# Kernel optimization log

Measured on AMD Instinct MI355X. Metric: run time of the kernel, lower is better.

Reference implementation:

```python
import jax, jax.numpy as jnp
import numpy as np

B, T, E, H = 2, 4096, 1024, 16
D = E // H
EPS = 1e-6


def setup_inputs() -> dict:
    key = jax.random.key(0)
    ks = jax.random.split(key, 9)
    s = 1.0 / np.sqrt(E)
    return {
        "x": jax.random.normal(ks[0], (B, T, E), dtype=jnp.float32),
        "wq": jax.random.uniform(ks[1], (E, E), jnp.float32, -s, s),
        "bq": jax.random.uniform(ks[2], (E,), jnp.float32, -s, s),
        "wk": jax.random.uniform(ks[3], (E, E), jnp.float32, -s, s),
        "bk": jax.random.uniform(ks[4], (E,), jnp.float32, -s, s),
        "wv": jax.random.uniform(ks[5], (E, E), jnp.float32, -s, s),
        "bv": jax.random.uniform(ks[6], (E,), jnp.float32, -s, s),
        "wo": jax.random.uniform(ks[7], (E, E), jnp.float32, -s, s),
        "bo": jax.random.uniform(ks[8], (E,), jnp.float32, -s, s),
    }


def _feature_map(x):
    # elu(x) + 1
    return jnp.where(x > 0, x + 1.0, jnp.exp(x))


def reference(x, wq, bq, wk, bk, wv, bv, wo, bo):
    b, t, e = x.shape
    q = _feature_map(x @ wq + bq).reshape(b, t, H, D)
    k = _feature_map(x @ wk + bk).reshape(b, t, H, D)
    v = (x @ wv + bv).reshape(b, t, H, D)

    # time-major for the recurrence: [T, B, H, D]
    qT = jnp.moveaxis(q, 1, 0)
    kT = jnp.moveaxis(k, 1, 0)
    vT = jnp.moveaxis(v, 1, 0)

    S0 = jnp.zeros((b, H, D, D), dtype=x.dtype)  # running sum of k \otimes v
    z0 = jnp.zeros((b, H, D), dtype=x.dtype)     # running sum of k

    def step(carry, qkv):
        S, z = carry
        qt, kt, vt = qkv
        S = S + jnp.einsum('bhd,bhe->bhde', kt, vt)
        z = z + kt
        num = jnp.einsum('bhd,bhde->bhe', qt, S)
        den = jnp.einsum('bhd,bhd->bh', qt, z)[..., None] + EPS
        return (S, z), num / den

    _, outT = jax.lax.scan(step, (S0, z0), (qT, kT, vT))  # [T, B, H, D]
    out = jnp.moveaxis(outT, 0, 1).reshape(b, t, e)
    return out @ wo + bo
```

## Files before the change

### kernel.cpp

```cpp
#include <hip/hip_runtime.h>
#include <hip/hip_bf16.h>
#include <cstdint>
#include <cstddef>

#define B_   2
#define T_   4096
#define E_   1024
#define H_   16
#define D_   64
#define M_   (B_ * T_)
#define KDIM 1024
#define NDIM 1024
#define EPSC 1e-6f
#define CT   128
#define NC   (T_ / CT)

typedef __attribute__((ext_vector_type(8))) short bf16x8;
typedef __attribute__((ext_vector_type(4))) float f32x4;

__device__ __forceinline__ float bf2f(uint32_t u) {
    union { uint32_t u; float f; } x; x.u = u << 16; return x.f;
}
__device__ __forceinline__ unsigned short f2bf(float f) {
    union { float f; uint32_t u; } x; x.f = f;
    uint32_t r = x.u + 0x7fffu + ((x.u >> 16) & 1u);
    return (unsigned short)(r >> 16);
}
__device__ __forceinline__ void gload16(const void* g, void* l) {
    __builtin_amdgcn_global_load_lds(
        (const __attribute__((address_space(1))) void*)g,
        (__attribute__((address_space(3))) void*)l, 16, 0, 0);
}

__global__ __launch_bounds__(256) void prep(
    const float* __restrict__ x, unsigned short* __restrict__ xb,
    const float* __restrict__ w0, const float* __restrict__ w1,
    const float* __restrict__ w2, const float* __restrict__ w3,
    unsigned short* __restrict__ o0, unsigned short* __restrict__ o1,
    unsigned short* __restrict__ o2, unsigned short* __restrict__ o3)
{
    const int t = threadIdx.x;
    if (blockIdx.z == 4) {
        const int bi = blockIdx.y * 16 + blockIdx.x;
        const float4* p = (const float4*)x;
#pragma unroll
        for (int j = 0; j < 16; ++j) {
            const int i = bi * 256 + t + j * 65536;
            float4 a = p[i * 2], b = p[i * 2 + 1];
            ushort4 q0 = make_ushort4(f2bf(a.x), f2bf(a.y), f2bf(a.z), f2bf(a.w));
            ushort4 q1 = make_ushort4(f2bf(b.x), f2bf(b.y), f2bf(b.z), f2bf(b.w));
            *(ushort4*)&xb[(size_t)i * 8] = q0;
            *(ushort4*)&xb[(size_t)i * 8 + 4] = q1;
        }
        return;
    }
    const float* src; unsigned short* dst;
    switch (blockIdx.z) {
        case 0: src = w0; dst = o0; break;
        case 1: src = w1; dst = o1; break;
        case 2: src = w2; dst = o2; break;
        default: src = w3; dst = o3; break;
    }
    __shared__ float tile[64][65];
    const int tx = t & 63, ty = t >> 6;
    const int r0 = blockIdx.y * 64, c0 = blockIdx.x * 64;
#pragma unroll
    for (int i = 0; i < 16; ++i)
        tile[ty + i * 4][tx] = src[(size_t)(r0 + ty + i * 4) * KDIM + c0 + tx];
    __syncthreads();
#pragma unroll
    for (int i = 0; i < 16; ++i)
        dst[(size_t)(c0 + ty + i * 4) * KDIM + r0 + tx] = f2bf(tile[tx][ty + i * 4]);
}

template <int MODE>
__global__ __launch_bounds__(512, 1) void gemm_tb(
    const unsigned short* __restrict__ A,
    const unsigned short* __restrict__ Wt,
    const float* __restrict__ bq, const float* __restrict__ bk,
    const float* __restrict__ bv,
    unsigned short* __restrict__ qb,  unsigned short* __restrict__ kb,
    unsigned short* __restrict__ ktb, unsigned short* __restrict__ vtb,
    float* __restrict__ outf)
{
    __shared__ char lds[147456];

    const int tid  = threadIdx.x;
    const int lane = tid & 63;
    const int w    = tid >> 6;
    const int wm   = w >> 1;
    const int wn   = w & 1;
    const int lo   = lane & 15, hi = lane >> 4;

    int bx, by;
    if (MODE == 0) {
        const int orig = blockIdx.x;
        const int swz  = (orig & 7) * 96 + (orig >> 3);
        bx = swz % 24;
        by = swz / 24;
    } else {
        const int orig = blockIdx.x;
        bx = orig & 7;
        by = orig >> 3;
    }
    const int row0 = by * 256;
    const int col0 = bx * 128;

    int sr, skE;
    { int X = tid * 16; int Y = X ^ (((X >> 7) & 7) << 4);
      sr = Y >> 7; skE = (Y & 127) >> 1; }
    const unsigned short* pa = A  + (size_t)(row0 + sr) * KDIM + skE;
    const unsigned short* pb = Wt + (size_t)(col0 + sr) * KDIM + skE;

#define STG(t, da, db) {                                                      \
    { char* d_ = (da) + tid * 16;                                             \
      _Pragma("unroll") for (int ch = 0; ch < 4; ++ch)                        \
        gload16(pa + (size_t)ch * 64 * KDIM + (t) * 64, d_ + ch * 8192); }    \
    { char* d_ = (db) + tid * 16;                                             \
      _Pragma("unroll") for (int ch = 0; ch < 2; ++ch)                        \
        gload16(pb + (size_t)ch * 64 * KDIM + (t) * 64, d_ + ch * 8192); } }

    const int koff0 = (hi * 16)       ^ ((lane & 7) << 4);
    const int koff1 = (64 + hi * 16)  ^ ((lane & 7) << 4);

    f32x4 acc[4][4] = {};
    const int NT = KDIM / 64;

    char* pA0 = lds;           char* pB0 = lds + 98304;
    char* pA1 = lds + 32768;   char* pB1 = lds + 114688;
    char* pA2 = lds + 65536;   char* pB2 = lds + 131072;

    STG(0, pA0, pB0);
    STG(1, pA1, pB1);
    asm volatile("s_waitcnt vmcnt(6)" ::: "memory");
    __builtin_amdgcn_s_barrier();

    for (int t = 0; t < NT; ++t) {
        if (t + 2 < NT) STG(t + 2, pA2, pB2);

        bf16x8 af[4][2], bfr[4][2];
#pragma unroll
        for (int m = 0; m < 4; ++m) {
            const char* p = pA0 + (wm * 64 + m * 16 + lo) * 128;
            af[m][0] = *(const bf16x8*)(p + koff0);
            af[m][1] = *(const bf16x8*)(p + koff1);
        }
#pragma unroll
        for (int n = 0; n < 4; ++n) {
            const char* p = pB0 + (wn * 64 + n * 16 + lo) * 128;
            bfr[n][0] = *(const bf16x8*)(p + koff0);
            bfr[n][1] = *(const bf16x8*)(p + koff1);
        }
        __builtin_amdgcn_s_setprio(1);
#pragma unroll
        for (int kk = 0; kk < 2; ++kk)
#pragma unroll
            for (int m = 0; m < 4; ++m)
#pragma unroll
                for (int n = 0; n < 4; ++n)
                    acc[m][n] = __builtin_amdgcn_mfma_f32_16x16x32_bf16(
                        af[m][kk], bfr[n][kk], acc[m][n], 0, 0, 0);
        __builtin_amdgcn_s_setprio(0);

        if (t + 2 < NT) { asm volatile("s_waitcnt vmcnt(6)" ::: "memory"); }
        else            { asm volatile("s_waitcnt vmcnt(0)" ::: "memory"); }
        asm volatile("s_waitcnt lgkmcnt(0)" ::: "memory");
        __builtin_amdgcn_s_barrier();

        char* ta = pA0; pA0 = pA1; pA1 = pA2; pA2 = ta;
        char* tb = pB0; pB0 = pB1; pB1 = pB2; pB2 = tb;
    }
#undef STG

    if (MODE == 1) {
#pragma unroll
        for (int n = 0; n < 4; ++n) {
            const int col = col0 + wn * 64 + n * 16 + lo;
            const float bval = bq[col];
#pragma unroll
            for (int m = 0; m < 4; ++m) {
                const int rbase = row0 + wm * 64 + m * 16 + hi * 4;
#pragma unroll
                for (int j = 0; j < 4; ++j)
                    outf[(size_t)(rbase + j) * NDIM + col] = acc[m][n][j] + bval;
            }
        }
        return;
    }

    unsigned short* ep = (unsigned short*)lds;
    const int matid = bx >> 3;
    const float* bias = (matid == 0) ? bq : (matid == 1) ? bk : bv;
#pragma unroll
    for (int n = 0; n < 4; ++n) {
        const int lcol = wn * 64 + n * 16 + lo;
        const float bval = bias[(bx & 7) * 128 + lcol];
#pragma unroll
        for (int m = 0; m < 4; ++m) {
            const int lr0 = wm * 64 + m * 16 + hi * 4;
#pragma unroll
            for (int j = 0; j < 4; ++j) {
                float v = acc[m][n][j] + bval;
                if (matid <= 1) v = (v > 0.f) ? (v + 1.f) : __expf(v);
                ep[(lr0 + j) * 136 + lcol] = f2bf(v);
            }
        }
    }
    __syncthreads();

    const int b   = row0 >> 12;
    const int tg0 = row0 & (T_ - 1);
    const int h0  = (bx & 7) * 2;

    if (matid <= 1) {
        unsigned short* dst0 = (matid == 0) ? qb : kb;
#pragma unroll
        for (int it = 0; it < 8; ++it) {
            const int vid = it * 512 + tid;
            const int head = vid >> 11;
            const int rem = vid & 2047;
            const int tr = rem >> 3, c8 = rem & 7;
            uint4 v = *(const uint4*)&ep[tr * 136 + head * 64 + c8 * 8];
            *(uint4*)&dst0[((size_t)((b * H_ + h0 + head) * T_) + tg0 + tr) * D_
                           + c8 * 8] = v;
        }
    }
    if (matid >= 1) {
        unsigned short* dstT = (matid == 1) ? ktb : vtb;
#pragma unroll
        for (int it = 0; it < 8; ++it) {
            const int vid = it * 512 + tid;
            const int head = vid >> 11;
            const int rem = vid & 2047;
            const int d = rem & 63, t8 = rem >> 6;
            unsigned short vals[8];
#pragma unroll
            for (int i = 0; i < 8; ++i)
                vals[i] = ep[(t8 * 8 + i) * 136 + head * 64 + d];
            *(uint4*)&dstT[((size_t)((b * H_ + h0 + head) * D_) + d) * T_
                           + tg0 + t8 * 8] = *(const uint4*)vals;
        }
    }
}

__global__ __launch_bounds__(256) void chunk_sums_mfma(
    const unsigned short* __restrict__ Kt,
    const unsigned short* __restrict__ Vt,
    unsigned short* __restrict__ Sl,
    unsigned short* __restrict__ Zl)
{
    const int tid = threadIdx.x, lane = tid & 63, w = tid >> 6;
    const int lo = lane & 15, hi = lane >> 4;
    const int cid = blockIdx.x, bh = cid >> 5, c = cid & 31, t0 = c * CT;
    const unsigned short* kT = Kt + (size_t)bh * 64 * T_ + t0;
    const unsigned short* vT = Vt + (size_t)bh * 64 * T_ + t0;

    const bf16x8 ones8 = {0x3F80, 0x3F80, 0x3F80, 0x3F80,
                          0x3F80, 0x3F80, 0x3F80, 0x3F80};
    f32x4 acc[5] = {};
#pragma unroll
    for (int kt = 0; kt < 4; ++kt) {
        bf16x8 af = *(const bf16x8*)&kT[(size_t)(w * 16 + lo) * T_ + kt * 32 + hi * 8];
        bf16x8 bfr[5];
#pragma unroll
        for (int et = 0; et < 4; ++et)
            bfr[et] = *(const bf16x8*)&vT[(size_t)(et * 16 + lo) * T_ + kt * 32 + hi * 8];
        bfr[4] = ones8;
#pragma unroll
        for (int et = 0; et < 5; ++et)
            acc[et] = __builtin_amdgcn_mfma_f32_16x16x32_bf16(af, bfr[et], acc[et], 0, 0, 0);
    }
    unsigned short* sO = Sl + (size_t)cid * 4096;
    const int d0 = w * 16 + hi * 4;
#pragma unroll
    for (int et = 0; et < 4; ++et) {
        const int e = et * 16 + lo;
        ushort4 pk = make_ushort4(f2bf(acc[et][0]), f2bf(acc[et][1]),
                                  f2bf(acc[et][2]), f2bf(acc[et][3]));
        *(ushort4*)&sO[e * 64 + d0] = pk;
    }
    if (lo == 0) {
        ushort4 pk = make_ushort4(f2bf(acc[4][0]), f2bf(acc[4][1]),
                                  f2bf(acc[4][2]), f2bf(acc[4][3]));
        *(ushort4*)&Zl[(size_t)cid * 64 + d0] = pk;
    }
}

__global__ __launch_bounds__(256) void chunk_scan_bf(
    unsigned short* __restrict__ S, unsigned short* __restrict__ Z)
{
    const int bh = blockIdx.y;
    const int f0 = blockIdx.x * 512 + threadIdx.x * 2;
    float a0 = 0.f, a1 = 0.f;
    unsigned short* base = S + (size_t)bh * NC * 4096 + f0;
    for (int c = 0; c < NC; ++c) {
        uint32_t* p = (uint32_t*)(base + (size_t)c * 4096);
        uint32_t v = *p;
        float c0 = bf2f(v & 0xffffu), c1 = bf2f(v >> 16);
        *p = (uint32_t)f2bf(a0) | ((uint32_t)f2bf(a1) << 16);
        a0 += c0; a1 += c1;
    }
    if (blockIdx.x == 0 && threadIdx.x < 32) {
        float b0 = 0.f, b1 = 0.f;
        unsigned short* zb = Z + (size_t)bh * NC * 64 + threadIdx.x * 2;
        for (int c = 0; c < NC; ++c) {
            uint32_t* p = (uint32_t*)(zb + (size_t)c * 64);
            uint32_t v = *p;
            float c0 = bf2f(v & 0xffffu), c1 = bf2f(v >> 16);
            *p = (uint32_t)f2bf(b0) | ((uint32_t)f2bf(b1) << 16);
            b0 += c0; b1 += c1;
        }
    }
}

__global__ __launch_bounds__(256) void chunk_attn_mfma(
    const unsigned short* __restrict__ Qb,
    const unsigned short* __restrict__ Kb,
    const unsigned short* __restrict__ Vt,
    const unsigned short* __restrict__ SpT,
    const unsigned short* __restrict__ Zp,
    unsigned short* __restrict__ att)
{
    __shared__ unsigned short lds[128 * 128];

    const int tid = threadIdx.x;
    const int lane = tid & 63;
    const int w = tid >> 6;
    const int lo = lane & 15, hi = lane >> 4;
    const int cid = blockIdx.x;
    const int bh = cid >> 5, c = cid & 31;
    const int t0 = c * CT;

    const unsigned short* qB = Qb + ((size_t)bh * T_ + t0) * 64;
    const unsigned short* kB = Kb + ((size_t)bh * T_ + t0) * 64;
    const unsigned short* vB = Vt + (size_t)bh * 64 * T_ + t0;
    const unsigned short* sB = SpT + (size_t)cid * 4096;
    const unsigned short* zB = Zp + (size_t)cid * 64;

    bf16x8 ka[2][2];
#pragma unroll
    for (int si = 0; si < 2; ++si)
#pragma unroll
        for (int kt = 0; kt < 2; ++kt)
            ka[si][kt] = *(const bf16x8*)&kB[(w * 32 + si * 16 + lo) * 64 + kt * 32 + hi * 8];

    f32x4 pacc[2][8] = {};
#pragma unroll
    for (int ti = 0; ti < 8; ++ti) {
        if (ti >= 2 * w) {
#pragma unroll
            for (int kt = 0; kt < 2; ++kt) {
                bf16x8 qf = *(const bf16x8*)&qB[(ti * 16 + lo) * 64 + kt * 32 + hi * 8];
                pacc[0][ti] = __builtin_amdgcn_mfma_f32_16x16x32_bf16(
                    ka[0][kt], qf, pacc[0][ti], 0, 0, 0);
                if (ti >= 2 * w + 1)
                    pacc[1][ti] = __builtin_amdgcn_mfma_f32_16x16x32_bf16(
                        ka[1][kt], qf, pacc[1][ti], 0, 0, 0);
            }
        }
    }
#pragma unroll
    for (int ti = 0; ti < 8; ++ti) {
        if (ti >= 2 * w) {
            const int t = ti * 16 + lo;
#pragma unroll
            for (int si = 0; si < 2; ++si) {
                const int s0 = w * 32 + si * 16 + hi * 4;
                ushort4 pk;
                unsigned short* pe = (unsigned short*)&pk;
#pragma unroll
                for (int j = 0; j < 4; ++j)
                    pe[j] = (s0 + j <= t) ? f2bf(pacc[si][ti][j]) : (unsigned short)0;
                *(ushort4*)((char*)lds + t * 256 + ((s0 * 2) ^ ((t & 7) << 4))) = pk;
            }
        }
    }
    __syncthreads();

    const bf16x8 ones8 = {0x3F80, 0x3F80, 0x3F80, 0x3F80,
                          0x3F80, 0x3F80, 0x3F80, 0x3F80};
    f32x4 acc[2][5] = {};
#pragma unroll
    for (int kt = 0; kt < 6; ++kt) {
        const int skt = kt - 2;
        if (kt < 2 || skt <= w) {
            bf16x8 bfr[5];
            if (kt < 2) {
#pragma unroll
                for (int et = 0; et < 4; ++et)
                    bfr[et] = *(const bf16x8*)&sB[(et * 16 + lo) * 64 + kt * 32 + hi * 8];
                bfr[4] = *(const bf16x8*)&zB[kt * 32 + hi * 8];
            } else {
#pragma unroll
                for (int et = 0; et < 4; ++et)
                    bfr[et] = *(const bf16x8*)&vB[(size_t)(et * 16 + lo) * T_ + skt * 32 + hi * 8];
                bfr[4] = ones8;
            }
#pragma unroll
            for (int m = 0; m < 2; ++m) {
                const int t = w * 32 + m * 16 + lo;
                bf16x8 af;
                if (kt < 2)
                    af = *(const bf16x8*)&qB[t * 64 + kt * 32 + hi * 8];
                else
                    af = *(const bf16x8*)((char*)lds + t * 256 +
                         (((skt * 32 + hi * 8) * 2) ^ ((t & 7) << 4)));
#pragma unroll
                for (int et = 0; et < 5; ++et)
                    acc[m][et] = __builtin_amdgcn_mfma_f32_16x16x32_bf16(
                        af, bfr[et], acc[m][et], 0, 0, 0);
            }
        }
    }

    __syncthreads();
#pragma unroll
    for (int m = 0; m < 2; ++m) {
#pragma unroll
        for (int j = 0; j < 4; ++j) {
            const int t = w * 32 + m * 16 + hi * 4 + j;
            const float rden = 1.f / (acc[m][4][j] + EPSC);
#pragma unroll
            for (int et = 0; et < 4; ++et) {
                const int e = et * 16 + lo;
                *(unsigned short*)((char*)lds + t * 144 + e * 2) =
                    f2bf(acc[m][et][j] * rden);
            }
        }
    }
    __syncthreads();
    const int b = bh >> 4, h = bh & 15;
#pragma unroll
    for (int r = 0; r < 4; ++r) {
        const int vid = tid + r * 256;
        const int t = vid >> 3, eg = vid & 7;
        uint4 val = *(const uint4*)((const char*)lds + t * 144 + eg * 16);
        *(uint4*)&att[(size_t)(b * T_ + t0 + t) * E_ + h * 64 + eg * 8] = val;
    }
}

extern "C" void kernel_launch(void* const* d_in, const int* in_sizes, int n_in,
                              void* d_out, int out_size, void* d_ws, size_t ws_size,
                              hipStream_t stream)
{
    const float* x  = (const float*)d_in[0];
    const float* wq = (const float*)d_in[1];
    const float* bq = (const float*)d_in[2];
    const float* wk = (const float*)d_in[3];
    const float* bk = (const float*)d_in[4];
    const float* wv = (const float*)d_in[5];
    const float* bv = (const float*)d_in[6];
    const float* wo = (const float*)d_in[7];
    const float* bo = (const float*)d_in[8];
    float* out = (float*)d_out;

    char* ws = (char*)d_ws;
    unsigned short* qb  = (unsigned short*)(ws);
    unsigned short* kb  = (unsigned short*)(ws + (size_t)16 * 1024 * 1024);
    unsigned short* ktb = (unsigned short*)(ws + (size_t)32 * 1024 * 1024);
    unsigned short* vtb = (unsigned short*)(ws + (size_t)48 * 1024 * 1024);
    unsigned short* xb  = (unsigned short*)(ws + (size_t)64 * 1024 * 1024);
    unsigned short* attb = xb;
    unsigned short* Sl  = (unsigned short*)(ws + (size_t)80 * 1024 * 1024);
    unsigned short* Zl  = (unsigned short*)(ws + (size_t)88 * 1024 * 1024);
    unsigned short* wqT = (unsigned short*)(ws + (size_t)88 * 1024 * 1024 + 128 * 1024);
    unsigned short* wkT = wqT + (size_t)KDIM * NDIM;
    unsigned short* wvT = wkT + (size_t)KDIM * NDIM;
    unsigned short* woT = wvT + (size_t)KDIM * NDIM;

    prep<<<dim3(16, 16, 5), 256, 0, stream>>>(x, xb, wq, wk, wv, wo,
                                              wqT, wkT, wvT, woT);

    gemm_tb<0><<<768, 512, 0, stream>>>(xb, wqT, bq, bk, bv,
                                        qb, kb, ktb, vtb, nullptr);

    chunk_sums_mfma<<<B_ * H_ * NC, 256, 0, stream>>>(ktb, vtb, Sl, Zl);
    chunk_scan_bf<<<dim3(8, B_ * H_), 256, 0, stream>>>(Sl, Zl);
    chunk_attn_mfma<<<B_ * H_ * NC, 256, 0, stream>>>(qb, kb, vtb, Sl, Zl, attb);

    gemm_tb<1><<<256, 512, 0, stream>>>(attb, woT, bo, nullptr, nullptr,
                                        nullptr, nullptr, nullptr, nullptr, out);
}
```

Measured before the change: 165.8 us.

## Use 256x256 tiles with 8-phase interleaved pipeline for QKV projection GEMM

Replaces the templated QKV GEMM with a dedicated kernel using 256x256 output tiles, eight warps in a 2x4 grid and double-buffered LDS. The main loop is split into four MFMA phases interleaved with partial global-to-LDS loads and barriers, and launch bounds now request two blocks per CU. The goal is more arithmetic per loaded byte and better overlap of loads with matrix math in the largest GEMM. The epilogue is done in two halves to fit LDS, and the output GEMM is split into its own plain kernel. Risks include register pressure from 32 accumulators per lane with occupancy 2, and the extra barriers.

```diff
diff --git a/kernel.cpp b/kernel.cpp
--- a/kernel.cpp
+++ b/kernel.cpp
@@ -73,15 +73,189 @@
         dst[(size_t)(c0 + ty + i * 4) * KDIM + r0 + tx] = f2bf(tile[tx][ty + i * 4]);
 }
 
-template <int MODE>
-__global__ __launch_bounds__(512, 1) void gemm_tb(
+__global__ __launch_bounds__(512, 2) void gemm_qkv8p(
     const unsigned short* __restrict__ A,
     const unsigned short* __restrict__ Wt,
     const float* __restrict__ bq, const float* __restrict__ bk,
     const float* __restrict__ bv,
     unsigned short* __restrict__ qb,  unsigned short* __restrict__ kb,
-    unsigned short* __restrict__ ktb, unsigned short* __restrict__ vtb,
-    float* __restrict__ outf)
+    unsigned short* __restrict__ ktb, unsigned short* __restrict__ vtb)
+{
+    __shared__ char lds[131072];
+
+    const int tid  = threadIdx.x;
+    const int lane = tid & 63;
+    const int w    = tid >> 6;
+    const int wm   = w >> 2;
+    const int wn   = w & 3;
+    const int lo   = lane & 15, hi = lane >> 4;
+
+    const int orig = blockIdx.x;
+    const int swz  = (orig & 7) * 48 + (orig >> 3);
+    const int bx = swz % 12;
+    const int by = swz / 12;
+    const int row0 = by * 256;
+    const int col0 = bx * 256;
+
+    const unsigned short* srcA[2][2];
+    const unsigned short* srcB[2][2];
+#pragma unroll
+    for (int h = 0; h < 2; ++h)
+#pragma unroll
+        for (int j = 0; j < 2; ++j) {
+            int X = j * 8192 + tid * 16;
+            int Y = X ^ (((X >> 7) & 7) << 4);
+            int lr = Y >> 7, ke = (Y & 127) >> 1;
+            srcA[h][j] = A  + (size_t)(row0 + h * 128 + lr) * KDIM + ke;
+            srcB[h][j] = Wt + (size_t)(col0 + h * 128 + lr) * KDIM + ke;
+        }
+
+#define STG_A(t, h) { char* d_ = lds + ((t) & 1) * 65536 + (h) * 16384 + tid * 16; \
+        gload16(srcA[h][0] + (t) * 64, d_); gload16(srcA[h][1] + (t) * 64, d_ + 8192); }
+#define STG_B(t, h) { char* d_ = lds + ((t) & 1) * 65536 + 32768 + (h) * 16384 + tid * 16; \
+        gload16(srcB[h][0] + (t) * 64, d_); gload16(srcB[h][1] + (t) * 64, d_ + 8192); }
+
+    const int koff0 = (hi * 16)      ^ ((lo & 7) << 4);
+    const int koff1 = (64 + hi * 16) ^ ((lo & 7) << 4);
+
+    f32x4  acc[8][4] = {};
+    bf16x8 af[4][2], bfr[4][2];
+    const int NT = KDIM / 64;
+
+#define MFMA16(mb, nb) {                                                      \
+    _Pragma("unroll") for (int kk = 0; kk < 2; ++kk)                          \
+    _Pragma("unroll") for (int m = 0; m < 4; ++m)                             \
+    _Pragma("unroll") for (int n = 0; n < 2; ++n)                             \
+        acc[(mb) + m][(nb) + n] = __builtin_amdgcn_mfma_f32_16x16x32_bf16(    \
+            af[m][kk], bfr[(nb) + n][kk], acc[(mb) + m][(nb) + n], 0, 0, 0); }
+
+    STG_A(0, 0); STG_A(0, 1); STG_B(0, 0); STG_B(0, 1);
+    STG_A(1, 0); STG_A(1, 1);
+    asm volatile("s_waitcnt vmcnt(4)" ::: "memory");
+    __builtin_amdgcn_s_barrier();
+
+    for (int t = 0; t < NT; ++t) {
+        const char* bb = lds + (t & 1) * 65536;
+        const char* bA = bb + wm * 16384;
+        const char* bB = bb + 32768 + (wn >> 1) * 16384;
+        const int lrb = (wn & 1) * 64;
+
+        if (t + 1 < NT) STG_B(t + 1, 0);
+#pragma unroll
+        for (int m = 0; m < 4; ++m) {
+            const char* p = bA + (m * 16 + lo) * 128;
+            af[m][0] = *(const bf16x8*)(p + koff0);
+            af[m][1] = *(const bf16x8*)(p + koff1);
+        }
+#pragma unroll
+        for (int n = 0; n < 4; ++n) {
+            const char* p = bB + (lrb + n * 16 + lo) * 128;
+            bfr[n][0] = *(const bf16x8*)(p + koff0);
+            bfr[n][1] = *(const bf16x8*)(p + koff1);
+        }
+        __builtin_amdgcn_s_barrier();
+        asm volatile("s_waitcnt lgkmcnt(0)" ::: "memory");
+        __builtin_amdgcn_s_setprio(1);
+        MFMA16(0, 0);
+        __builtin_amdgcn_s_setprio(0);
+        __builtin_amdgcn_s_barrier();
+
+        if (t + 1 < NT) STG_B(t + 1, 1);
+        __builtin_amdgcn_s_barrier();
+        __builtin_amdgcn_s_setprio(1);
+        MFMA16(0, 2);
+        __builtin_amdgcn_s_setprio(0);
+        __builtin_amdgcn_s_barrier();
+
+#pragma unroll
+        for (int m = 0; m < 4; ++m) {
+            const char* p = bA + ((m + 4) * 16 + lo) * 128;
+            af[m][0] = *(const bf16x8*)(p + koff0);
+            af[m][1] = *(const bf16x8*)(p + koff1);
+        }
+        __builtin_amdgcn_s_barrier();
+        asm volatile("s_waitcnt lgkmcnt(0)" ::: "memory");
+        __builtin_amdgcn_s_setprio(1);
+        MFMA16(4, 0);
+        __builtin_amdgcn_s_setprio(0);
+        __builtin_amdgcn_s_barrier();
+
+        if (t + 2 < NT) { STG_A(t + 2, 0); STG_A(t + 2, 1); }
+        __builtin_amdgcn_s_setprio(1);
+        MFMA16(4, 2);
+        __builtin_amdgcn_s_setprio(0);
+        if (t + 2 < NT)      asm volatile("s_waitcnt vmcnt(4)" ::: "memory");
+        else if (t + 1 < NT) asm volatile("s_waitcnt vmcnt(0)" ::: "memory");
+        __builtin_amdgcn_s_barrier();
+    }
+#undef STG_A
+#undef STG_B
+#undef MFMA16
+
+    unsigned short* ep = (unsigned short*)lds;
+    const int matid = bx >> 2;
+    const float* bias = (matid == 0) ? bq : (matid == 1) ? bk : bv;
+    const int b   = row0 >> 12;
+    const int tg0 = row0 & (T_ - 1);
+    const int h0  = (bx & 3) * 4;
+
+#pragma unroll
+    for (int ph = 0; ph < 2; ++ph) {
+        if (wm == ph) {
+#pragma unroll
+            for (int n = 0; n < 4; ++n) {
+                const int col = wn * 64 + n * 16 + lo;
+                const float bval = bias[(bx & 3) * 256 + col];
+#pragma unroll
+                for (int m = 0; m < 8; ++m) {
+#pragma unroll
+                    for (int j = 0; j < 4; ++j) {
+                        float v = acc[m][n][j] + bval;
+                        if (matid <= 1) v = (v > 0.f) ? (v + 1.f) : __expf(v);
+                        ep[(m * 16 + hi * 4 + j) * 272 + col] = f2bf(v);
+                    }
+                }
+            }
+        }
+        __syncthreads();
+
+        if (matid <= 1) {
+            unsigned short* dst0 = (matid == 0) ? qb : kb;
+#pragma unroll
+            for (int it = 0; it < 8; ++it) {
+                const int vid = it * 512 + tid;
+                const int r = vid >> 5;
+                const int lc8 = vid & 31;
+                const int head = lc8 >> 3, d8 = lc8 & 7;
+                uint4 v = *(const uint4*)&ep[r * 272 + lc8 * 8];
+                *(uint4*)&dst0[((size_t)((b * H_ + h0 + head) * T_)
+                                + tg0 + ph * 128 + r) * D_ + d8 * 8] = v;
+            }
+        }
+        if (matid >= 1) {
+            unsigned short* dstT = (matid == 1) ? ktb : vtb;
+#pragma unroll
+            for (int it = 0; it < 8; ++it) {
+                const int vid = it * 512 + tid;
+                const int d = vid & 63;
+                const int idx = vid >> 6;
+                const int head = idx >> 4, t8 = idx & 15;
+                unsigned short vals[8];
+#pragma unroll
+                for (int i = 0; i < 8; ++i)
+                    vals[i] = ep[(t8 * 8 + i) * 272 + head * 64 + d];
+                *(uint4*)&dstT[((size_t)((b * H_ + h0 + head) * D_) + d) * T_
+                               + tg0 + ph * 128 + t8 * 8] = *(const uint4*)vals;
+            }
+        }
+        __syncthreads();
+    }
+}
+
+__global__ __launch_bounds__(512, 1) void gemm_out_tb(
+    const unsigned short* __restrict__ A,
+    const unsigned short* __restrict__ Wt,
+    const float* __restrict__ bias, float* __restrict__ outf)
 {
     __shared__ char lds[147456];
 
@@ -92,17 +266,9 @@
     const int wn   = w & 1;
     const int lo   = lane & 15, hi = lane >> 4;
 
-    int bx, by;
-    if (MODE == 0) {
-        const int orig = blockIdx.x;
-        const int swz  = (orig & 7) * 96 + (orig >> 3);
-        bx = swz % 24;
-        by = swz / 24;
-    } else {
-        const int orig = blockIdx.x;
-        bx = orig & 7;
-        by = orig >> 3;
-    }
+    const int orig = blockIdx.x;
+    const int bx = orig & 7;
+    const int by = orig >> 3;
     const int row0 = by * 256;
     const int col0 = bx * 128;
 
@@ -172,73 +338,16 @@
     }
 #undef STG
 
-    if (MODE == 1) {
-#pragma unroll
-        for (int n = 0; n < 4; ++n) {
-            const int col = col0 + wn * 64 + n * 16 + lo;
-            const float bval = bq[col];
-#pragma unroll
-            for (int m = 0; m < 4; ++m) {
-                const int rbase = row0 + wm * 64 + m * 16 + hi * 4;
-#pragma unroll
-                for (int j = 0; j < 4; ++j)
-                    outf[(size_t)(rbase + j) * NDIM + col] = acc[m][n][j] + bval;
-            }
-        }
-        return;
-    }
-
-    unsigned short* ep = (unsigned short*)lds;
-    const int matid = bx >> 3;
-    const float* bias = (matid == 0) ? bq : (matid == 1) ? bk : bv;
 #pragma unroll
     for (int n = 0; n < 4; ++n) {
-        const int lcol = wn * 64 + n * 16 + lo;
-        const float bval = bias[(bx & 7) * 128 + lcol];
+        const int col = col0 + wn * 64 + n * 16 + lo;
+        const float bval = bias[col];
 #pragma unroll
         for (int m = 0; m < 4; ++m) {
-            const int lr0 = wm * 64 + m * 16 + hi * 4;
-#pragma unroll
-            for (int j = 0; j < 4; ++j) {
-                float v = acc[m][n][j] + bval;
-                if (matid <= 1) v = (v > 0.f) ? (v + 1.f) : __expf(v);
-                ep[(lr0 + j) * 136 + lcol] = f2bf(v);
-            }
-        }
-    }
-    __syncthreads();
-
-    const int b   = row0 >> 12;
-    const int tg0 = row0 & (T_ - 1);
-    const int h0  = (bx & 7) * 2;
-
-    if (matid <= 1) {
-        unsigned short* dst0 = (matid == 0) ? qb : kb;
-#pragma unroll
-        for (int it = 0; it < 8; ++it) {
-            const int vid = it * 512 + tid;
-            const int head = vid >> 11;
-            const int rem = vid & 2047;
-            const int tr = rem >> 3, c8 = rem & 7;
-            uint4 v = *(const uint4*)&ep[tr * 136 + head * 64 + c8 * 8];
-            *(uint4*)&dst0[((size_t)((b * H_ + h0 + head) * T_) + tg0 + tr) * D_
-                           + c8 * 8] = v;
-        }
-    }
-    if (matid >= 1) {
-        unsigned short* dstT = (matid == 1) ? ktb : vtb;
-#pragma unroll
-        for (int it = 0; it < 8; ++it) {
-            const int vid = it * 512 + tid;
-            const int head = vid >> 11;
-            const int rem = vid & 2047;
-            const int d = rem & 63, t8 = rem >> 6;
-            unsigned short vals[8];
-#pragma unroll
-            for (int i = 0; i < 8; ++i)
-                vals[i] = ep[(t8 * 8 + i) * 136 + head * 64 + d];
-            *(uint4*)&dstT[((size_t)((b * H_ + h0 + head) * D_) + d) * T_
-                           + tg0 + t8 * 8] = *(const uint4*)vals;
+            const int rbase = row0 + wm * 64 + m * 16 + hi * 4;
+#pragma unroll
+            for (int j = 0; j < 4; ++j)
+                outf[(size_t)(rbase + j) * NDIM + col] = acc[m][n][j] + bval;
         }
     }
 }
@@ -471,13 +580,11 @@
     prep<<<dim3(16, 16, 5), 256, 0, stream>>>(x, xb, wq, wk, wv, wo,
                                               wqT, wkT, wvT, woT);
 
-    gemm_tb<0><<<768, 512, 0, stream>>>(xb, wqT, bq, bk, bv,
-                                        qb, kb, ktb, vtb, nullptr);
+    gemm_qkv8p<<<384, 512, 0, stream>>>(xb, wqT, bq, bk, bv, qb, kb, ktb, vtb);
 
     chunk_sums_mfma<<<B_ * H_ * NC, 256, 0, stream>>>(ktb, vtb, Sl, Zl);
     chunk_scan_bf<<<dim3(8, B_ * H_), 256, 0, stream>>>(Sl, Zl);
     chunk_attn_mfma<<<B_ * H_ * NC, 256, 0, stream>>>(qb, kb, vtb, Sl, Zl, attb);
 
-    gemm_tb<1><<<256, 512, 0, stream>>>(attb, woT, bo, nullptr, nullptr,
-                                        nullptr, nullptr, nullptr, nullptr, out);
-}
+    gemm_out_tb<<<256, 512, 0, stream>>>(attb, woT, bo, out);
+}
```

Measured after the change: 175.5 us. 1.06x slower.

## Replace LDS-staged triple-buffered GEMM with direct global-to-register MFMA GEMM

Applied to the files above, without the earlier changes.

The QKV and output projection GEMMs stop staging A and W tiles through LDS with a triple-buffered global_load_lds pipeline. Each wave now loads its MFMA fragments straight from global memory into registers, on 128x128 tiles with 256 threads, which doubles the block count and allows more blocks per CU. The aim is to drop LDS traffic, barriers and waitcnt stalls and lean on L1/L2 and occupancy to hide latency. The cost is that operands shared across waves are no longer reused through LDS, so global and cache traffic rise, and the loop has no explicit prefetch.

```diff
diff --git a/kernel.cpp b/kernel.cpp
--- a/kernel.cpp
+++ b/kernel.cpp
@@ -26,11 +26,6 @@
     uint32_t r = x.u + 0x7fffu + ((x.u >> 16) & 1u);
     return (unsigned short)(r >> 16);
 }
-__device__ __forceinline__ void gload16(const void* g, void* l) {
-    __builtin_amdgcn_global_load_lds(
-        (const __attribute__((address_space(1))) void*)g,
-        (__attribute__((address_space(3))) void*)l, 16, 0, 0);
-}
 
 __global__ __launch_bounds__(256) void prep(
     const float* __restrict__ x, unsigned short* __restrict__ xb,
@@ -74,7 +69,7 @@
 }
 
 template <int MODE>
-__global__ __launch_bounds__(512, 1) void gemm_tb(
+__global__ __launch_bounds__(256) void gemm_reg(
     const unsigned short* __restrict__ A,
     const unsigned short* __restrict__ Wt,
     const float* __restrict__ bq, const float* __restrict__ bk,
@@ -83,75 +78,54 @@
     unsigned short* __restrict__ ktb, unsigned short* __restrict__ vtb,
     float* __restrict__ outf)
 {
-    __shared__ char lds[147456];
+    __shared__ unsigned short ep[(MODE == 0) ? 128 * 136 : 16];
 
     const int tid  = threadIdx.x;
     const int lane = tid & 63;
     const int w    = tid >> 6;
-    const int wm   = w >> 1;
-    const int wn   = w & 1;
+    const int wr   = w >> 1;
+    const int wc   = w & 1;
     const int lo   = lane & 15, hi = lane >> 4;
 
     int bx, by;
     if (MODE == 0) {
         const int orig = blockIdx.x;
-        const int swz  = (orig & 7) * 96 + (orig >> 3);
+        const int swz  = (orig & 7) * 192 + (orig >> 3);
         bx = swz % 24;
         by = swz / 24;
     } else {
         const int orig = blockIdx.x;
-        bx = orig & 7;
-        by = orig >> 3;
-    }
-    const int row0 = by * 256;
+        const int swz  = (orig & 7) * 64 + (orig >> 3);
+        bx = swz & 7;
+        by = swz >> 3;
+    }
+    const int row0 = by * 128;
     const int col0 = bx * 128;
 
-    int sr, skE;
-    { int X = tid * 16; int Y = X ^ (((X >> 7) & 7) << 4);
-      sr = Y >> 7; skE = (Y & 127) >> 1; }
-    const unsigned short* pa = A  + (size_t)(row0 + sr) * KDIM + skE;
-    const unsigned short* pb = Wt + (size_t)(col0 + sr) * KDIM + skE;
-
-#define STG(t, da, db) {                                                      \
-    { char* d_ = (da) + tid * 16;                                             \
-      _Pragma("unroll") for (int ch = 0; ch < 4; ++ch)                        \
-        gload16(pa + (size_t)ch * 64 * KDIM + (t) * 64, d_ + ch * 8192); }    \
-    { char* d_ = (db) + tid * 16;                                             \
-      _Pragma("unroll") for (int ch = 0; ch < 2; ++ch)                        \
-        gload16(pb + (size_t)ch * 64 * KDIM + (t) * 64, d_ + ch * 8192); } }
-
-    const int koff0 = (hi * 16)       ^ ((lane & 7) << 4);
-    const int koff1 = (64 + hi * 16)  ^ ((lane & 7) << 4);
+    const unsigned short* aP[4];
+    const unsigned short* bP[4];
+#pragma unroll
+    for (int m = 0; m < 4; ++m)
+        aP[m] = A + (size_t)(row0 + wr * 64 + m * 16 + lo) * KDIM + hi * 8;
+#pragma unroll
+    for (int n = 0; n < 4; ++n)
+        bP[n] = Wt + (size_t)(col0 + wc * 64 + n * 16 + lo) * KDIM + hi * 8;
 
     f32x4 acc[4][4] = {};
-    const int NT = KDIM / 64;
-
-    char* pA0 = lds;           char* pB0 = lds + 98304;
-    char* pA1 = lds + 32768;   char* pB1 = lds + 114688;
-    char* pA2 = lds + 65536;   char* pB2 = lds + 131072;
-
-    STG(0, pA0, pB0);
-    STG(1, pA1, pB1);
-    asm volatile("s_waitcnt vmcnt(6)" ::: "memory");
-    __builtin_amdgcn_s_barrier();
-
-    for (int t = 0; t < NT; ++t) {
-        if (t + 2 < NT) STG(t + 2, pA2, pB2);
-
+
+    for (int t = 0; t < KDIM / 64; ++t) {
         bf16x8 af[4][2], bfr[4][2];
+        const int ko = t * 64;
 #pragma unroll
         for (int m = 0; m < 4; ++m) {
-            const char* p = pA0 + (wm * 64 + m * 16 + lo) * 128;
-            af[m][0] = *(const bf16x8*)(p + koff0);
-            af[m][1] = *(const bf16x8*)(p + koff1);
+            af[m][0] = *(const bf16x8*)(aP[m] + ko);
+            af[m][1] = *(const bf16x8*)(aP[m] + ko + 32);
         }
 #pragma unroll
         for (int n = 0; n < 4; ++n) {
-            const char* p = pB0 + (wn * 64 + n * 16 + lo) * 128;
-            bfr[n][0] = *(const bf16x8*)(p + koff0);
-            bfr[n][1] = *(const bf16x8*)(p + koff1);
-        }
-        __builtin_amdgcn_s_setprio(1);
+            bfr[n][0] = *(const bf16x8*)(bP[n] + ko);
+            bfr[n][1] = *(const bf16x8*)(bP[n] + ko + 32);
+        }
 #pragma unroll
         for (int kk = 0; kk < 2; ++kk)
 #pragma unroll
@@ -160,26 +134,16 @@
                 for (int n = 0; n < 4; ++n)
                     acc[m][n] = __builtin_amdgcn_mfma_f32_16x16x32_bf16(
                         af[m][kk], bfr[n][kk], acc[m][n], 0, 0, 0);
-        __builtin_amdgcn_s_setprio(0);
-
-        if (t + 2 < NT) { asm volatile("s_waitcnt vmcnt(6)" ::: "memory"); }
-        else            { asm volatile("s_waitcnt vmcnt(0)" ::: "memory"); }
-        asm volatile("s_waitcnt lgkmcnt(0)" ::: "memory");
-        __builtin_amdgcn_s_barrier();
-
-        char* ta = pA0; pA0 = pA1; pA1 = pA2; pA2 = ta;
-        char* tb = pB0; pB0 = pB1; pB1 = pB2; pB2 = tb;
-    }
-#undef STG
+    }
 
     if (MODE == 1) {
 #pragma unroll
         for (int n = 0; n < 4; ++n) {
-            const int col = col0 + wn * 64 + n * 16 + lo;
+            const int col = col0 + wc * 64 + n * 16 + lo;
             const float bval = bq[col];
 #pragma unroll
             for (int m = 0; m < 4; ++m) {
-                const int rbase = row0 + wm * 64 + m * 16 + hi * 4;
+                const int rbase = row0 + wr * 64 + m * 16 + hi * 4;
 #pragma unroll
                 for (int j = 0; j < 4; ++j)
                     outf[(size_t)(rbase + j) * NDIM + col] = acc[m][n][j] + bval;
@@ -188,16 +152,15 @@
         return;
     }
 
-    unsigned short* ep = (unsigned short*)lds;
     const int matid = bx >> 3;
     const float* bias = (matid == 0) ? bq : (matid == 1) ? bk : bv;
 #pragma unroll
     for (int n = 0; n < 4; ++n) {
-        const int lcol = wn * 64 + n * 16 + lo;
+        const int lcol = wc * 64 + n * 16 + lo;
         const float bval = bias[(bx & 7) * 128 + lcol];
 #pragma unroll
         for (int m = 0; m < 4; ++m) {
-            const int lr0 = wm * 64 + m * 16 + hi * 4;
+            const int lr0 = wr * 64 + m * 16 + hi * 4;
 #pragma unroll
             for (int j = 0; j < 4; ++j) {
                 float v = acc[m][n][j] + bval;
@@ -216,9 +179,9 @@
         unsigned short* dst0 = (matid == 0) ? qb : kb;
 #pragma unroll
         for (int it = 0; it < 8; ++it) {
-            const int vid = it * 512 + tid;
-            const int head = vid >> 11;
-            const int rem = vid & 2047;
+            const int vid = it * 256 + tid;
+            const int head = vid >> 10;
+            const int rem = vid & 1023;
             const int tr = rem >> 3, c8 = rem & 7;
             uint4 v = *(const uint4*)&ep[tr * 136 + head * 64 + c8 * 8];
             *(uint4*)&dst0[((size_t)((b * H_ + h0 + head) * T_) + tg0 + tr) * D_
@@ -229,10 +192,10 @@
         unsigned short* dstT = (matid == 1) ? ktb : vtb;
 #pragma unroll
         for (int it = 0; it < 8; ++it) {
-            const int vid = it * 512 + tid;
-            const int head = vid >> 11;
-            const int rem = vid & 2047;
-            const int d = rem & 63, t8 = rem >> 6;
+            const int vid = it * 256 + tid;
+            const int d = vid & 63;
+            const int idx = vid >> 6;
+            const int head = idx >> 4, t8 = idx & 15;
             unsigned short vals[8];
 #pragma unroll
             for (int i = 0; i < 8; ++i)
@@ -471,13 +434,13 @@
     prep<<<dim3(16, 16, 5), 256, 0, stream>>>(x, xb, wq, wk, wv, wo,
                                               wqT, wkT, wvT, woT);
 
-    gemm_tb<0><<<768, 512, 0, stream>>>(xb, wqT, bq, bk, bv,
-                                        qb, kb, ktb, vtb, nullptr);
+    gemm_reg<0><<<1536, 256, 0, stream>>>(xb, wqT, bq, bk, bv,
+                                          qb, kb, ktb, vtb, nullptr);
 
     chunk_sums_mfma<<<B_ * H_ * NC, 256, 0, stream>>>(ktb, vtb, Sl, Zl);
     chunk_scan_bf<<<dim3(8, B_ * H_), 256, 0, stream>>>(Sl, Zl);
     chunk_attn_mfma<<<B_ * H_ * NC, 256, 0, stream>>>(qb, kb, vtb, Sl, Zl, attb);
 
-    gemm_tb<1><<<256, 512, 0, stream>>>(attb, woT, bo, nullptr, nullptr,
-                                        nullptr, nullptr, nullptr, nullptr, out);
-}
+    gemm_reg<1><<<512, 256, 0, stream>>>(attb, woT, bo, nullptr, nullptr,
+                                         nullptr, nullptr, nullptr, nullptr, out);
+}
```

After: 311.6 us. +87.9%, slower.
